# Kernel optimization log

Measured on AMD Instinct MI355X. Metric: run time of the kernel, lower is better.

## Reference

```python
import jax, jax.numpy as jnp
import numpy as np
from jax import lax

B, N, HID = 2, 2048, 2048
H, KVH, D = 16, 4, 128           # heads, kv heads, head_dim
GROUPS = H // KVH
FLA_WEIGHT = 0.01
NEG = -1e30


def setup_inputs() -> dict:
    key = jax.random.key(0)
    ks = jax.random.split(key, 5)
    s = 0.02
    return {
        "hidden_states": jax.random.normal(ks[0], (B, N, HID), jnp.float32),
        "Wq": jax.random.normal(ks[1], (HID, H * D), jnp.float32) * s,
        "Wk": jax.random.normal(ks[2], (HID, KVH * D), jnp.float32) * s,
        "Wv": jax.random.normal(ks[3], (HID, KVH * D), jnp.float32) * s,
        "Wo": jax.random.normal(ks[4], (H * D, HID), jnp.float32) * s,
    }


def _split_heads(x, h):
    b, n, _ = x.shape
    return x.reshape(b, n, h, -1).transpose(0, 2, 1, 3)  # b h n d


def _gla_attention(q, k, v, scale):
    # Gated linear attention: S_t = sigmoid(k_t) (.) S_{t-1} + k_t (x) v_t,
    # o_t = scale * q_t . S_t ; sequential recurrence over the seq dim.
    qs = jnp.moveaxis(q, 2, 0)  # n b h d
    ks = jnp.moveaxis(k, 2, 0)
    vs = jnp.moveaxis(v, 2, 0)

    def step(S, inp):
        qt, kt, vt = inp                                   # each (b,h,d)
        g = jax.nn.sigmoid(kt)                             # per-key-dim gate
        S = S * g[..., None] + kt[..., None] * vt[..., None, :]  # (b,h,d,dv)
        ot = scale * jnp.einsum('bhd,bhde->bhe', qt, S)
        return S, ot

    S0 = jnp.zeros(q.shape[:2] + (q.shape[-1], v.shape[-1]), q.dtype)
    _, o = lax.scan(step, S0, (qs, ks, vs))                # n b h dv
    return jnp.moveaxis(o, 0, 2)                           # b h n dv


def reference(hidden_states, Wq, Wk, Wv, Wo):
    scale = 1.0 / np.sqrt(D)
    q = _split_heads(hidden_states @ Wq, H)                # b h n d
    k = _split_heads(hidden_states @ Wk, KVH)
    v = _split_heads(hidden_states @ Wv, KVH)
    k = jnp.repeat(k, GROUPS, axis=1)                      # repeat_kv -> b H n d
    v = jnp.repeat(v, GROUPS, axis=1)

    # FLA branch
    fla = _gla_attention(q, k, v, scale)                   # b h n d
    fla = fla.transpose(0, 2, 1, 3).reshape(B, N, H * D)   # b n (h d)

    # Base causal softmax attention
    scores = jnp.einsum('bhnd,bhmd->bhnm', q, k) * scale
    causal = jnp.tril(jnp.ones((N, N), bool))
    scores = jnp.where(causal, scores, NEG)
    attn = jax.nn.softmax(scores, axis=-1)
    base = jnp.einsum('bhnm,bhmd->bhnd', attn, v)
    base = base.transpose(0, 2, 1, 3).reshape(B, N, H * D) @ Wo

    return base + FLA_WEIGHT * fla
```

## Files before the change

### kernel.cpp

```cpp
#include <hip/hip_runtime.h>
#include <hip/hip_bf16.h>
#include <cstdint>
#include <cstddef>


typedef __attribute__((ext_vector_type(4))) float f32x4;
typedef __attribute__((ext_vector_type(2))) float f32x2;
typedef __attribute__((ext_vector_type(8))) short s16x8;
typedef unsigned short u16;
typedef unsigned int u32;

__device__ __forceinline__ float bfu2f(u16 u) {
  union { unsigned int i; float f; } x; x.i = ((unsigned int)u) << 16; return x.f;
}
__device__ __forceinline__ u16 f2bfu(float f) {
  union { float f; unsigned int i; } x; x.f = f;
  unsigned int r = x.i + 0x7fffu + ((x.i >> 16) & 1u);
  return (u16)(r >> 16);
}
__device__ __forceinline__ void bf8_to_f(s16x8 v, float* o) {
  union { s16x8 v; u16 u[8]; } x; x.v = v;
#pragma unroll
  for (int j = 0; j < 8; j++) o[j] = bfu2f(x.u[j]);
}
__device__ __forceinline__ s16x8 pack_bf8(f32x4 lo, f32x4 hi) {
  union { s16x8 v; u16 u[8]; } x;
#pragma unroll
  for (int j = 0; j < 4; j++) { x.u[j] = f2bfu(lo[j]); x.u[4 + j] = f2bfu(hi[j]); }
  return x.v;
}
__device__ __forceinline__ void gload_lds16(const u16* g, u16* l) {
  __builtin_amdgcn_global_load_lds(
      (__attribute__((address_space(1))) void*)(g),
      (__attribute__((address_space(3))) void*)(l), 16, 0, 0);
}

__global__ __launch_bounds__(256) void f32_to_bf16(
    const float* __restrict__ src, u16* __restrict__ dst, int n8) {
  const int i = blockIdx.x * 256 + threadIdx.x;
  if (i < n8) {
    f32x4 a = *(const f32x4*)(src + (size_t)i * 8);
    f32x4 b = *(const f32x4*)(src + (size_t)i * 8 + 4);
    *(s16x8*)(dst + (size_t)i * 8) = pack_bf8(a, b);
  }
}

__global__ __launch_bounds__(256) void transpose_f32_bf16(
    const float* __restrict__ src, u16* __restrict__ dst, int R, int C) {
  __shared__ u16 tile[32][33];
  const int bx = blockIdx.x * 32, by = blockIdx.y * 32;
  const int tx = threadIdx.x & 31, ty = threadIdx.x >> 5;
#pragma unroll
  for (int i = 0; i < 32; i += 8)
    tile[ty + i][tx] = f2bfu(src[(size_t)(by + ty + i) * C + bx + tx]);
  __syncthreads();
#pragma unroll
  for (int i = 0; i < 32; i += 8)
    dst[(size_t)(bx + ty + i) * R + by + tx] = tile[tx][ty + i];
}

__global__ __launch_bounds__(256) void transpose_bf16(
    const u16* __restrict__ src, u16* __restrict__ dst, int R, int C) {
  __shared__ u16 tile[32][33];
  const int bx = blockIdx.x * 32, by = blockIdx.y * 32;
  const int tx = threadIdx.x & 31, ty = threadIdx.x >> 5;
#pragma unroll
  for (int i = 0; i < 32; i += 8)
    tile[ty + i][tx] = src[(size_t)(by + ty + i) * C + bx + tx];
  __syncthreads();
#pragma unroll
  for (int i = 0; i < 32; i += 8)
    dst[(size_t)(bx + ty + i) * R + by + tx] = tile[tx][ty + i];
}

__device__ __forceinline__ void gemm_core_256x128(
    const u16* __restrict__ A, const u16* __restrict__ Bt,
    int m0, int n0, int K, int Nst,
    u16* __restrict__ Cb, float* __restrict__ Cf,
    const u16* __restrict__ addsrc, float addw,
    u16* Abuf, u16* Bbuf) {
  const int t = threadIdx.x, w = t >> 6, l = t & 63, lm = l & 15, lq = l >> 4;
  const int wr = w >> 1, wc = w & 1;
  const int tr = t >> 3, tc8 = (t & 7) * 8;
  const f32x4 z4 = {0.f, 0.f, 0.f, 0.f};
  f32x4 acc[4][4];
#pragma unroll
  for (int i = 0; i < 4; i++)
#pragma unroll
    for (int j = 0; j < 4; j++) acc[i][j] = z4;
  const u16* Ag = A + (size_t)m0 * K;
  const u16* Bg = Bt + (size_t)n0 * K;
  auto stage = [&](int kt, int bufi) {
#pragma unroll
    for (int i = 0; i < 4; i++) {
      const int row = i * 64 + tr;
      const int col = tc8 ^ ((row & 7) << 3);
      gload_lds16(Ag + (size_t)row * K + kt * 64 + col,
                  Abuf + bufi * 16384 + i * 4096 + w * 512);
    }
#pragma unroll
    for (int i = 0; i < 2; i++) {
      const int row = i * 64 + tr;
      const int col = tc8 ^ ((row & 7) << 3);
      gload_lds16(Bg + (size_t)row * K + kt * 64 + col,
                  Bbuf + bufi * 8192 + i * 4096 + w * 512);
    }
  };
  const int nt = K >> 6;
  stage(0, 0);
  int cur = 0;
#pragma unroll 1
  for (int kt = 0; kt < nt; kt++) {
    if (kt + 1 < nt) {
      stage(kt + 1, cur ^ 1);
      asm volatile("s_waitcnt vmcnt(6)" ::: "memory");
    } else {
      asm volatile("s_waitcnt vmcnt(0)" ::: "memory");
    }
    __builtin_amdgcn_s_barrier();
    const u16* Ab = Abuf + cur * 16384;
    const u16* Bb = Bbuf + cur * 8192;
    s16x8 af[4][2], bff[4][2];
#pragma unroll
    for (int sm = 0; sm < 4; sm++) {
      const int row = wr * 64 + sm * 16 + lm;
#pragma unroll
      for (int kk = 0; kk < 2; kk++)
        af[sm][kk] = *(const s16x8*)&Ab[row * 64 +
            ((((kk << 6) | (lq << 4)) ^ ((row & 7) << 4)) >> 1)];
    }
#pragma unroll
    for (int sn = 0; sn < 4; sn++) {
      const int row = wc * 64 + sn * 16 + lm;
#pragma unroll
      for (int kk = 0; kk < 2; kk++)
        bff[sn][kk] = *(const s16x8*)&Bb[row * 64 +
            ((((kk << 6) | (lq << 4)) ^ ((row & 7) << 4)) >> 1)];
    }
#pragma unroll
    for (int kk = 0; kk < 2; kk++)
#pragma unroll
      for (int sm = 0; sm < 4; sm++)
#pragma unroll
        for (int sn = 0; sn < 4; sn++)
          acc[sm][sn] = __builtin_amdgcn_mfma_f32_16x16x32_bf16(
              af[sm][kk], bff[sn][kk], acc[sm][sn], 0, 0, 0);
    asm volatile("s_waitcnt lgkmcnt(0)" ::: "memory");
    __builtin_amdgcn_s_barrier();
    cur ^= 1;
  }
#pragma unroll
  for (int sm = 0; sm < 4; sm++)
#pragma unroll
    for (int sn = 0; sn < 4; sn++)
#pragma unroll
      for (int r = 0; r < 4; r++) {
        const int row = m0 + wr * 64 + sm * 16 + lq * 4 + r;
        const int col = n0 + wc * 64 + sn * 16 + lm;
        float v = acc[sm][sn][r];
        if (Cf) {
          if (addsrc) v += addw * bfu2f(addsrc[(size_t)row * Nst + col]);
          Cf[(size_t)row * Nst + col] = v;
        } else {
          Cb[(size_t)row * Nst + col] = f2bfu(v);
        }
      }
}

__global__ __launch_bounds__(512) void gemm_qkv2(
    const u16* __restrict__ A, const u16* __restrict__ WqT, const u16* __restrict__ WkT,
    const u16* __restrict__ WvT, u16* __restrict__ Qo, u16* __restrict__ Ko,
    u16* __restrict__ Vo) {
  __shared__ u16 Abuf[2 * 16384];
  __shared__ u16 Bbuf[2 * 8192];
  int f = blockIdx.y * 24 + blockIdx.x;
  f = (f & 7) * 48 + (f >> 3);
  const int by = f / 24, bx = f - by * 24;
  const u16* Bt; u16* Cb; int n0, Nst;
  if (bx < 16)      { Bt = WqT; Cb = Qo; n0 = bx * 128;        Nst = 2048; }
  else if (bx < 20) { Bt = WkT; Cb = Ko; n0 = (bx - 16) * 128; Nst = 512; }
  else              { Bt = WvT; Cb = Vo; n0 = (bx - 20) * 128; Nst = 512; }
  gemm_core_256x128(A, Bt, by * 256, n0, 2048, Nst, Cb, nullptr, nullptr, 0.f,
                    Abuf, Bbuf);
}

__global__ __launch_bounds__(512) void gemm_out2(
    const u16* __restrict__ A, const u16* __restrict__ Bt, float* __restrict__ Cf,
    const u16* __restrict__ addsrc) {
  __shared__ u16 Abuf[2 * 16384];
  __shared__ u16 Bbuf[2 * 8192];
  int f = blockIdx.y * 16 + blockIdx.x;
  f = (f & 7) * 32 + (f >> 3);
  const int by = f >> 4, bx = f & 15;
  gemm_core_256x128(A, Bt, by * 256, bx * 128, 2048, 2048, nullptr, Cf,
                    addsrc, 0.01f, Abuf, Bbuf);
}

__global__ __launch_bounds__(512) void flash_attn_wave(
    const u16* __restrict__ Q, const u16* __restrict__ Kx,
    const u16* __restrict__ Vt, u16* __restrict__ AO) {
  __shared__ u16 Klds[2][64 * 128];
  __shared__ u16 Vlds[2][128 * 64];
  __shared__ u16 Pl[8][16][68];
  const int bid = blockIdx.x;
  const int set = bid & 7;
  const int b = set >> 2, kvh = set & 3;
  const int rest = bid >> 3;
  const int j0 = rest >> 1, hp = rest & 1;
  const int t = threadIdx.x, w = t >> 6, l = t & 63, lm = l & 15, lq = l >> 4;
  const int h = kvh * 4 + hp * 2 + (w & 1);
  const int cs = (w >> 1) & 1, mh = w >> 2;
  const float scale = 0.0883883476483184f;
  const u16* Kbase = Kx + (size_t)(b * 2048) * 512 + kvh * 128;
  const u16* Vbase = Vt + (size_t)(b * 512 + kvh * 128) * 2048;
  const f32x4 z4 = {0.f, 0.f, 0.f, 0.f};

  auto stage = [&](int kt, int bufi) {
    const int key0 = kt * 64;
#pragma unroll
    for (int r = 0; r < 2; r++) {
      const int row = r * 32 + w * 4 + (l >> 4);
      const int scb = ((l & 15) * 16) ^ ((row & 7) << 4);
      gload_lds16(Kbase + (size_t)(key0 + row) * 512 + (scb >> 1),
                  &Klds[bufi][r * 4096 + w * 512]);
    }
#pragma unroll
    for (int r = 0; r < 2; r++) {
      const int row = r * 64 + w * 8 + (l >> 3);
      const int scb = ((l & 7) * 16) ^ ((row & 7) << 4);
      gload_lds16(Vbase + (size_t)row * 2048 + key0 + (scb >> 1),
                  &Vlds[bufi][r * 4096 + w * 512]);
    }
  };

#pragma unroll 1
  for (int ph = 0; ph < 2; ph++) {
    const int j = ph ? (31 - j0) : j0;
    const int c = 2 * j + cs;
    const int base = c * 32;
    int cur = 0;
    stage(0, 0);
    s16x8 qf[4];
#pragma unroll
    for (int kk = 0; kk < 4; kk++)
      qf[kk] = *(const s16x8*)(Q + ((size_t)(b * 2048 + base + mh * 16 + lm)) * 2048 +
                               h * 128 + kk * 32 + lq * 8);
    f32x4 oacc[8];
#pragma unroll
    for (int e = 0; e < 8; e++) oacc[e] = z4;
    float lsum[4] = {0.f, 0.f, 0.f, 0.f};
#pragma unroll 1
    for (int kt = 0; kt <= j; kt++) {
      const int key0 = kt * 64;
      if (kt < j) {
        stage(kt + 1, cur ^ 1);
        asm volatile("s_waitcnt vmcnt(4)" ::: "memory");
      } else {
        asm volatile("s_waitcnt vmcnt(0)" ::: "memory");
      }
      __builtin_amdgcn_s_barrier();
      const char* KB = (const char*)&Klds[cur][0];
      const char* VB = (const char*)&Vlds[cur][0];
      s16x8 kf[4][4];
#pragma unroll
      for (int nst = 0; nst < 4; nst++)
#pragma unroll
        for (int kk = 0; kk < 4; kk++) {
          const int row = nst * 16 + lm;
          const int cb = (kk * 64 + lq * 16) ^ ((row & 7) << 4);
          kf[nst][kk] = *(const s16x8*)(KB + row * 256 + cb);
        }
      f32x4 sacc[4];
#pragma unroll
      for (int i = 0; i < 4; i++) sacc[i] = z4;
#pragma unroll
      for (int nst = 0; nst < 4; nst++)
#pragma unroll
        for (int kk = 0; kk < 4; kk++)
          sacc[nst] = __builtin_amdgcn_mfma_f32_16x16x32_bf16(
              qf[kk], kf[nst][kk], sacc[nst], 0, 0, 0);
      const bool diag = (kt == j);
#pragma unroll
      for (int r = 0; r < 4; r++) {
        const int qrow = base + mh * 16 + lq * 4 + r;
#pragma unroll
        for (int nst = 0; nst < 4; nst++) {
          float pv = __expf(sacc[nst][r] * scale);
          if (diag && (key0 + nst * 16 + lm > qrow)) pv = 0.f;
          lsum[r] += pv;
          Pl[w][lq * 4 + r][nst * 16 + lm] = f2bfu(pv);
        }
      }
      s16x8 vf[8][2];
#pragma unroll
      for (int et = 0; et < 8; et++)
#pragma unroll
        for (int kc = 0; kc < 2; kc++) {
          const int row = et * 16 + lm;
          const int cb = (kc * 64 + lq * 16) ^ ((row & 7) << 4);
          vf[et][kc] = *(const s16x8*)(VB + row * 128 + cb);
        }
      s16x8 pf[2];
#pragma unroll
      for (int kc = 0; kc < 2; kc++)
        pf[kc] = *(const s16x8*)&Pl[w][lm][kc * 32 + lq * 8];
#pragma unroll
      for (int et = 0; et < 8; et++)
#pragma unroll
        for (int kc = 0; kc < 2; kc++)
          oacc[et] = __builtin_amdgcn_mfma_f32_16x16x32_bf16(
              pf[kc], vf[et][kc], oacc[et], 0, 0, 0);
      asm volatile("s_waitcnt lgkmcnt(0)" ::: "memory");
      __builtin_amdgcn_s_barrier();
      cur ^= 1;
    }
#pragma unroll
    for (int r = 0; r < 4; r++) {
#pragma unroll
      for (int off = 1; off < 16; off <<= 1)
        lsum[r] += __shfl_xor(lsum[r], off, 64);
    }
#pragma unroll
    for (int r = 0; r < 4; r++) {
      const float inv = 1.f / lsum[r];
      const int row = base + mh * 16 + lq * 4 + r;
      u16* op = AO + ((size_t)(b * 2048 + row)) * 2048 + h * 128;
#pragma unroll
      for (int et = 0; et < 8; et++) op[et * 16 + lm] = f2bfu(oacc[et][r] * inv);
    }
  }
}

__global__ __launch_bounds__(256) void fla_contrib32(
    const u16* __restrict__ Kx, const u16* __restrict__ Vt,
    u16* __restrict__ Gg, u16* __restrict__ Ktg, u16* __restrict__ MT,
    float* __restrict__ Lam) {
  __shared__ float gl[32][132];
  __shared__ float kl[32][132];
  __shared__ float ktl[32][132];
  __shared__ u16 khT[128][40];
  const int c = blockIdx.x, kvh = blockIdx.y, b = blockIdx.z;
  const int bk = b * 4 + kvh;
  const int t = threadIdx.x;
  const size_t cb = (size_t)bk * 64 + c;
  {
    const int r = t >> 3, c0 = (t & 7) * 16;
    const u16* kp = Kx + ((size_t)(b * 2048 + c * 32 + r)) * 512 + kvh * 128 + c0;
#pragma unroll
    for (int i = 0; i < 2; i++) {
      float kv[8];
      bf8_to_f(*(const s16x8*)(kp + i * 8), kv);
#pragma unroll
      for (int j = 0; j < 8; j++) {
        kl[r][c0 + i * 8 + j] = kv[j];
        gl[r][c0 + i * 8 + j] = 1.f / (1.f + __expf(-kv[j]));
      }
    }
  }
  __syncthreads();
  if (t < 128) {
    float G = 1.f;
#pragma unroll
    for (int s = 0; s < 32; s++) {
      G *= gl[s][t];
      gl[s][t] = G;
      ktl[s][t] = kl[s][t] / G;
    }
    Lam[cb * 128 + t] = G;
    const float lam = G;
#pragma unroll
    for (int s = 0; s < 32; s++) khT[t][s] = f2bfu(ktl[s][t] * lam);
  }
  __syncthreads();
  {
    const int r = t >> 3, c0 = (t & 7) * 16;
    u16* gp = Gg + cb * 4096 + r * 128 + c0;
    u16* kp = Ktg + cb * 4096 + r * 128 + c0;
#pragma unroll
    for (int i = 0; i < 2; i++) {
      f32x4 a = *(f32x4*)&gl[r][c0 + i * 8];
      f32x4 b2 = *(f32x4*)&gl[r][c0 + i * 8 + 4];
      *(s16x8*)(gp + i * 8) = pack_bf8(a, b2);
      a = *(f32x4*)&ktl[r][c0 + i * 8];
      b2 = *(f32x4*)&ktl[r][c0 + i * 8 + 4];
      *(s16x8*)(kp + i * 8) = pack_bf8(a, b2);
    }
  }
  const int w = t >> 6, l = t & 63, lm = l & 15, lq = l >> 4;
  const f32x4 z4 = {0.f, 0.f, 0.f, 0.f};
  f32x4 macc[2][8];
#pragma unroll
  for (int ei = 0; ei < 2; ei++)
#pragma unroll
    for (int dt = 0; dt < 8; dt++) macc[ei][dt] = z4;
  s16x8 vtf[2];
#pragma unroll
  for (int ei = 0; ei < 2; ei++) {
    const int et = w * 2 + ei;
    vtf[ei] = *(const s16x8*)(Vt + ((size_t)(b * 512 + kvh * 128 + et * 16 + lm)) * 2048 +
                              c * 32 + lq * 8);
  }
#pragma unroll
  for (int dt = 0; dt < 8; dt++) {
    s16x8 kf = *(const s16x8*)&khT[dt * 16 + lm][lq * 8];
#pragma unroll
    for (int ei = 0; ei < 2; ei++)
      macc[ei][dt] = __builtin_amdgcn_mfma_f32_16x16x32_bf16(vtf[ei], kf, macc[ei][dt], 0, 0, 0);
  }
  u16* mp = MT + cb * 16384;
#pragma unroll
  for (int ei = 0; ei < 2; ei++)
#pragma unroll
    for (int dt = 0; dt < 8; dt++)
#pragma unroll
      for (int r = 0; r < 4; r++)
        mp[(size_t)((w * 2 + ei) * 16 + lq * 4 + r) * 128 + dt * 16 + lm] =
            f2bfu(macc[ei][dt][r]);
}

__global__ __launch_bounds__(256) void fla_prefix32(
    const u16* __restrict__ MT, const float* __restrict__ Lam, u16* __restrict__ SwsT) {
  const int eg = blockIdx.x, bk = blockIdx.y;
  const int t = threadIdx.x;
  const int e = eg * 4 + (t >> 6), d0 = (t & 63) * 2;
  const size_t cb0 = (size_t)bk * 64;
  const u16* mp = MT + cb0 * 16384 + e * 128 + d0;
  const float* lp = Lam + cb0 * 128 + d0;
  u16* sp = SwsT + cb0 * 16384 + e * 128 + d0;
  float s0 = 0.f, s1 = 0.f;
  u32 mnext = *(const u32*)mp;
  f32x2 lnext = *(const f32x2*)lp;
#pragma unroll 1
  for (int c = 0; c < 64; c++) {
    const u32 mcur = mnext;
    const f32x2 lcur = lnext;
    if (c < 63) {
      mnext = *(const u32*)(mp + (size_t)(c + 1) * 16384);
      lnext = *(const f32x2*)(lp + (size_t)(c + 1) * 128);
    }
    *(u32*)(sp + (size_t)c * 16384) = (u32)f2bfu(s0) | ((u32)f2bfu(s1) << 16);
    s0 = s0 * lcur[0] + bfu2f((u16)(mcur & 0xffffu));
    s1 = s1 * lcur[1] + bfu2f((u16)(mcur >> 16));
  }
}

__global__ __launch_bounds__(256) void fla_output_mfma(
    const u16* __restrict__ Q, const u16* __restrict__ Gg, const u16* __restrict__ Ktg,
    const u16* __restrict__ SwsT, const u16* __restrict__ Vt, u16* __restrict__ Fla) {
  __shared__ u16 Pl[4][2][16][40];
  const int c = blockIdx.x, h = blockIdx.y, b = blockIdx.z;
  const int kvh = h >> 2, bk = b * 4 + kvh;
  const int t = threadIdx.x, w = t >> 6, l = t & 63, lm = l & 15, lq = l >> 4;
  const float scale = 0.0883883476483184f;
  const size_t cb = (size_t)bk * 64 + c;
  const f32x4 z4 = {0.f, 0.f, 0.f, 0.f};
  s16x8 qgf[2][4];
#pragma unroll
  for (int m = 0; m < 2; m++)
#pragma unroll
    for (int kk = 0; kk < 4; kk++) {
      float qv[8], gv[8];
      bf8_to_f(*(const s16x8*)(Q + ((size_t)(b * 2048 + c * 32 + m * 16 + lm)) * 2048 +
                               h * 128 + kk * 32 + lq * 8), qv);
      bf8_to_f(*(const s16x8*)(Gg + cb * 4096 + (m * 16 + lm) * 128 + kk * 32 + lq * 8), gv);
      f32x4 a, b2;
#pragma unroll
      for (int j = 0; j < 4; j++) { a[j] = qv[j] * gv[j]; b2[j] = qv[4 + j] * gv[4 + j]; }
      qgf[m][kk] = pack_bf8(a, b2);
    }
  f32x4 sacc[2][2];
#pragma unroll
  for (int m = 0; m < 2; m++)
#pragma unroll
    for (int st = 0; st < 2; st++) sacc[m][st] = z4;
#pragma unroll
  for (int st = 0; st < 2; st++)
#pragma unroll
    for (int kk = 0; kk < 4; kk++) {
      s16x8 ktf = *(const s16x8*)(Ktg + cb * 4096 + (st * 16 + lm) * 128 + kk * 32 + lq * 8);
#pragma unroll
      for (int m = 0; m < 2; m++)
        sacc[m][st] = __builtin_amdgcn_mfma_f32_16x16x32_bf16(qgf[m][kk], ktf, sacc[m][st], 0, 0, 0);
    }
#pragma unroll
  for (int m = 0; m < 2; m++)
#pragma unroll
    for (int st = 0; st < 2; st++)
#pragma unroll
      for (int r = 0; r < 4; r++) {
        const int trow = m * 16 + lq * 4 + r;
        const int scol = st * 16 + lm;
        Pl[w][m][lq * 4 + r][st * 16 + lm] = f2bfu(scol <= trow ? sacc[m][st][r] : 0.f);
      }
  s16x8 pf[2];
#pragma unroll
  for (int m = 0; m < 2; m++) pf[m] = *(const s16x8*)&Pl[w][m][lm][lq * 8];
  f32x4 oacc[2][2];
#pragma unroll
  for (int m = 0; m < 2; m++)
#pragma unroll
    for (int ei = 0; ei < 2; ei++) oacc[m][ei] = z4;
#pragma unroll
  for (int ei = 0; ei < 2; ei++) {
    const int et = w * 2 + ei;
    s16x8 vtf = *(const s16x8*)(Vt + ((size_t)(b * 512 + kvh * 128 + et * 16 + lm)) * 2048 +
                                c * 32 + lq * 8);
#pragma unroll
    for (int m = 0; m < 2; m++)
      oacc[m][ei] = __builtin_amdgcn_mfma_f32_16x16x32_bf16(pf[m], vtf, oacc[m][ei], 0, 0, 0);
#pragma unroll
    for (int kk = 0; kk < 4; kk++) {
      s16x8 s0f = *(const s16x8*)(SwsT + cb * 16384 + (et * 16 + lm) * 128 + kk * 32 + lq * 8);
#pragma unroll
      for (int m = 0; m < 2; m++)
        oacc[m][ei] = __builtin_amdgcn_mfma_f32_16x16x32_bf16(qgf[m][kk], s0f, oacc[m][ei], 0, 0, 0);
    }
  }
#pragma unroll
  for (int m = 0; m < 2; m++)
#pragma unroll
    for (int ei = 0; ei < 2; ei++)
#pragma unroll
      for (int r = 0; r < 4; r++)
        Fla[((size_t)(b * 2048 + c * 32 + m * 16 + lq * 4 + r)) * 2048 + h * 128 +
            (w * 2 + ei) * 16 + lm] = f2bfu(scale * oacc[m][ei][r]);
}

extern "C" void kernel_launch(void* const* d_in, const int* in_sizes, int n_in,
                              void* d_out, int out_size, void* d_ws, size_t ws_size,
                              hipStream_t stream) {
  const float* X  = (const float*)d_in[0];
  const float* Wq = (const float*)d_in[1];
  const float* Wk = (const float*)d_in[2];
  const float* Wv = (const float*)d_in[3];
  const float* Wo = (const float*)d_in[4];
  float* out = (float*)d_out;

  char* ws = (char*)d_ws;
  size_t off = 0;
  auto alloc = [&](size_t bytes) { void* p = ws + off; off += (bytes + 255) & ~(size_t)255; return p; };
  u16* WoT = (u16*)alloc(2048ull * 2048 * 2);
  u16* Qb  = (u16*)alloc(4096ull * 2048 * 2);
  u16* Kb  = (u16*)alloc(4096ull * 512 * 2);
  u16* Vb  = (u16*)alloc(4096ull * 512 * 2);
  u16* Vtb = (u16*)alloc(2ull * 512 * 2048 * 2);
  u16* Fla = (u16*)alloc(4096ull * 2048 * 2);
  u16* SH16 = (u16*)alloc(4096ull * 2048 * 2);
  u16* Xb = SH16;
  u16* MT = SH16;
  u16* AO = SH16;
  char* BIG = (char*)alloc(26ull * 1024 * 1024);
  u16* WqT = (u16*)BIG;
  u16* WkT = (u16*)(BIG + 8ull * 1024 * 1024);
  u16* WvT = (u16*)(BIG + 10ull * 1024 * 1024);
  u16* Gg   = (u16*)BIG;
  u16* Ktg  = (u16*)(BIG + 4194304ull);
  u16* SwsT = (u16*)(BIG + 8388608ull);
  float* Lam = (float*)(BIG + 8388608ull + 16777216ull);
  (void)ws_size; (void)in_sizes; (void)n_in; (void)out_size;

  dim3 blk(256);
  f32_to_bf16<<<dim3(4096), blk, 0, stream>>>(X, Xb, 4096 * 2048 / 8);
  transpose_f32_bf16<<<dim3(64, 64), blk, 0, stream>>>(Wq, WqT, 2048, 2048);
  transpose_f32_bf16<<<dim3(16, 64), blk, 0, stream>>>(Wk, WkT, 2048, 512);
  transpose_f32_bf16<<<dim3(16, 64), blk, 0, stream>>>(Wv, WvT, 2048, 512);
  transpose_f32_bf16<<<dim3(64, 64), blk, 0, stream>>>(Wo, WoT, 2048, 2048);

  gemm_qkv2<<<dim3(24, 16), dim3(512), 0, stream>>>(Xb, WqT, WkT, WvT, Qb, Kb, Vb);

  transpose_bf16<<<dim3(16, 64), blk, 0, stream>>>(Vb, Vtb, 2048, 512);
  transpose_bf16<<<dim3(16, 64), blk, 0, stream>>>(Vb + 2048ull * 512, Vtb + 512ull * 2048, 2048, 512);

  fla_contrib32<<<dim3(64, 4, 2), blk, 0, stream>>>(Kb, Vtb, Gg, Ktg, MT, Lam);
  fla_prefix32<<<dim3(32, 8), blk, 0, stream>>>(MT, Lam, SwsT);
  fla_output_mfma<<<dim3(64, 16, 2), blk, 0, stream>>>(Qb, Gg, Ktg, SwsT, Vtb, Fla);

  flash_attn_wave<<<dim3(256), dim3(512), 0, stream>>>(Qb, Kb, Vtb, AO);

  gemm_out2<<<dim3(16, 16), dim3(512), 0, stream>>>(AO, WoT, out, Fla);
}
```

Baseline: 396.6 us.

## Replace QKV GEMM with simple 128x128 kernel and triple-buffer output GEMM

The QKV projection now uses a new 256-thread 128x128-tile kernel with a single LDS buffer, K-step 32, unswizzled layout and no tile-order remapping. It replaces the 512-thread 256x128 double-buffered swizzled path. The output GEMM is inlined and switched to a 3-stage LDS pipeline, with two stages prefetched, to hide more load latency. The simpler QKV kernel loses prefetch overlap and swizzling and may hit LDS bank conflicts. The triple buffer raises LDS use and may lower occupancy.

```diff
diff --git a/kernel.cpp b/kernel.cpp
--- a/kernel.cpp
+++ b/kernel.cpp
@@ -73,12 +73,72 @@
     dst[(size_t)(bx + ty + i) * R + by + tx] = tile[tx][ty + i];
 }
 
-__device__ __forceinline__ void gemm_core_256x128(
-    const u16* __restrict__ A, const u16* __restrict__ Bt,
-    int m0, int n0, int K, int Nst,
-    u16* __restrict__ Cb, float* __restrict__ Cf,
-    const u16* __restrict__ addsrc, float addw,
-    u16* Abuf, u16* Bbuf) {
+__global__ __launch_bounds__(256) void gemm_qkv(
+    const u16* __restrict__ A, const u16* __restrict__ WqT, const u16* __restrict__ WkT,
+    const u16* __restrict__ WvT, u16* __restrict__ Qo, u16* __restrict__ Ko,
+    u16* __restrict__ Vo) {
+  __shared__ u16 Al[128 * 32];
+  __shared__ u16 Bl[128 * 32];
+  const int bx = blockIdx.x;
+  const u16* Bt; u16* Cb; int n0, Nst;
+  if (bx < 16)      { Bt = WqT; Cb = Qo; n0 = bx * 128;        Nst = 2048; }
+  else if (bx < 20) { Bt = WkT; Cb = Ko; n0 = (bx - 16) * 128; Nst = 512; }
+  else              { Bt = WvT; Cb = Vo; n0 = (bx - 20) * 128; Nst = 512; }
+  const int K = 2048;
+  const int m0 = blockIdx.y * 128;
+  const int t = threadIdx.x, w = t >> 6, l = t & 63, lm = l & 15, lq = l >> 4;
+  const int wr = w >> 1, wc = w & 1;
+  const f32x4 z4 = {0.f, 0.f, 0.f, 0.f};
+  f32x4 acc[4][4];
+#pragma unroll
+  for (int i = 0; i < 4; i++)
+#pragma unroll
+    for (int j = 0; j < 4; j++) acc[i][j] = z4;
+  const int srow = l >> 2, scol = (l & 3) * 8;
+  const u16* Ag = A + (size_t)(m0 + w * 32 + srow) * K + scol;
+  const u16* Bg = Bt + (size_t)(n0 + w * 32 + srow) * K + scol;
+  u16* Alw = &Al[(w * 32) * 32];
+  u16* Blw = &Bl[(w * 32) * 32];
+  for (int kk = 0; kk < K; kk += 32) {
+    gload_lds16(Ag + kk, Alw);
+    gload_lds16(Ag + (size_t)16 * K + kk, Alw + 16 * 32);
+    gload_lds16(Bg + kk, Blw);
+    gload_lds16(Bg + (size_t)16 * K + kk, Blw + 16 * 32);
+    __syncthreads();
+    s16x8 af[4], bfr[4];
+#pragma unroll
+    for (int sm = 0; sm < 4; sm++) af[sm] = *(const s16x8*)&Al[(wr * 64 + sm * 16 + lm) * 32 + lq * 8];
+#pragma unroll
+    for (int sn = 0; sn < 4; sn++) bfr[sn] = *(const s16x8*)&Bl[(wc * 64 + sn * 16 + lm) * 32 + lq * 8];
+#pragma unroll
+    for (int sm = 0; sm < 4; sm++)
+#pragma unroll
+      for (int sn = 0; sn < 4; sn++)
+        acc[sm][sn] = __builtin_amdgcn_mfma_f32_16x16x32_bf16(af[sm], bfr[sn], acc[sm][sn], 0, 0, 0);
+    __syncthreads();
+  }
+#pragma unroll
+  for (int sm = 0; sm < 4; sm++)
+#pragma unroll
+    for (int sn = 0; sn < 4; sn++)
+#pragma unroll
+      for (int r = 0; r < 4; r++) {
+        const int row = m0 + wr * 64 + sm * 16 + lq * 4 + r;
+        const int col = n0 + wc * 64 + sn * 16 + lm;
+        Cb[(size_t)row * Nst + col] = f2bfu(acc[sm][sn][r]);
+      }
+}
+
+__global__ __launch_bounds__(512) void gemm_out2(
+    const u16* __restrict__ A, const u16* __restrict__ Bt, float* __restrict__ Cf,
+    const u16* __restrict__ addsrc) {
+  __shared__ u16 Abuf[3 * 16384];
+  __shared__ u16 Bbuf[3 * 8192];
+  int f = blockIdx.y * 16 + blockIdx.x;
+  f = (f & 7) * 32 + (f >> 3);
+  const int by = f >> 4, bx = f & 15;
+  const int m0 = by * 256, n0 = bx * 128;
+  const int K = 2048, Nst = 2048;
   const int t = threadIdx.x, w = t >> 6, l = t & 63, lm = l & 15, lq = l >> 4;
   const int wr = w >> 1, wc = w & 1;
   const int tr = t >> 3, tc8 = (t & 7) * 8;
@@ -108,11 +168,15 @@
   };
   const int nt = K >> 6;
   stage(0, 0);
+  stage(1, 1);
   int cur = 0;
 #pragma unroll 1
   for (int kt = 0; kt < nt; kt++) {
-    if (kt + 1 < nt) {
-      stage(kt + 1, cur ^ 1);
+    if (kt + 2 < nt) {
+      int nb = cur + 2; if (nb >= 3) nb -= 3;
+      stage(kt + 2, nb);
+      asm volatile("s_waitcnt vmcnt(12)" ::: "memory");
+    } else if (kt + 1 < nt) {
       asm volatile("s_waitcnt vmcnt(6)" ::: "memory");
     } else {
       asm volatile("s_waitcnt vmcnt(0)" ::: "memory");
@@ -147,7 +211,7 @@
               af[sm][kk], bff[sn][kk], acc[sm][sn], 0, 0, 0);
     asm volatile("s_waitcnt lgkmcnt(0)" ::: "memory");
     __builtin_amdgcn_s_barrier();
-    cur ^= 1;
+    cur = (cur == 2) ? 0 : cur + 1;
   }
 #pragma unroll
   for (int sm = 0; sm < 4; sm++)
@@ -157,43 +221,9 @@
       for (int r = 0; r < 4; r++) {
         const int row = m0 + wr * 64 + sm * 16 + lq * 4 + r;
         const int col = n0 + wc * 64 + sn * 16 + lm;
-        float v = acc[sm][sn][r];
-        if (Cf) {
-          if (addsrc) v += addw * bfu2f(addsrc[(size_t)row * Nst + col]);
-          Cf[(size_t)row * Nst + col] = v;
-        } else {
-          Cb[(size_t)row * Nst + col] = f2bfu(v);
-        }
+        float v = acc[sm][sn][r] + 0.01f * bfu2f(addsrc[(size_t)row * Nst + col]);
+        Cf[(size_t)row * Nst + col] = v;
       }
-}
-
-__global__ __launch_bounds__(512) void gemm_qkv2(
-    const u16* __restrict__ A, const u16* __restrict__ WqT, const u16* __restrict__ WkT,
-    const u16* __restrict__ WvT, u16* __restrict__ Qo, u16* __restrict__ Ko,
-    u16* __restrict__ Vo) {
-  __shared__ u16 Abuf[2 * 16384];
-  __shared__ u16 Bbuf[2 * 8192];
-  int f = blockIdx.y * 24 + blockIdx.x;
-  f = (f & 7) * 48 + (f >> 3);
-  const int by = f / 24, bx = f - by * 24;
-  const u16* Bt; u16* Cb; int n0, Nst;
-  if (bx < 16)      { Bt = WqT; Cb = Qo; n0 = bx * 128;        Nst = 2048; }
-  else if (bx < 20) { Bt = WkT; Cb = Ko; n0 = (bx - 16) * 128; Nst = 512; }
-  else              { Bt = WvT; Cb = Vo; n0 = (bx - 20) * 128; Nst = 512; }
-  gemm_core_256x128(A, Bt, by * 256, n0, 2048, Nst, Cb, nullptr, nullptr, 0.f,
-                    Abuf, Bbuf);
-}
-
-__global__ __launch_bounds__(512) void gemm_out2(
-    const u16* __restrict__ A, const u16* __restrict__ Bt, float* __restrict__ Cf,
-    const u16* __restrict__ addsrc) {
-  __shared__ u16 Abuf[2 * 16384];
-  __shared__ u16 Bbuf[2 * 8192];
-  int f = blockIdx.y * 16 + blockIdx.x;
-  f = (f & 7) * 32 + (f >> 3);
-  const int by = f >> 4, bx = f & 15;
-  gemm_core_256x128(A, Bt, by * 256, bx * 128, 2048, 2048, nullptr, Cf,
-                    addsrc, 0.01f, Abuf, Bbuf);
 }
 
 __global__ __launch_bounds__(512) void flash_attn_wave(
@@ -566,7 +596,7 @@
   transpose_f32_bf16<<<dim3(16, 64), blk, 0, stream>>>(Wv, WvT, 2048, 512);
   transpose_f32_bf16<<<dim3(64, 64), blk, 0, stream>>>(Wo, WoT, 2048, 2048);
 
-  gemm_qkv2<<<dim3(24, 16), dim3(512), 0, stream>>>(Xb, WqT, WkT, WvT, Qb, Kb, Vb);
+  gemm_qkv<<<dim3(24, 32), blk, 0, stream>>>(Xb, WqT, WkT, WvT, Qb, Kb, Vb);
 
   transpose_bf16<<<dim3(16, 64), blk, 0, stream>>>(Vb, Vtb, 2048, 512);
   transpose_bf16<<<dim3(16, 64), blk, 0, stream>>>(Vb + 2048ull * 512, Vtb + 512ull * 2048, 2048, 512);
```

Result: faster. 363.6 us (-8.3%).
